# Performance work log

Hardware: AMD Instinct MI355X
Metric: run time of the kernel (lower is better)

Reference implementation:

```python
import jax, jax.numpy as jnp
import numpy as np

PAD = 1  # symmetric spatial padding (pad_H == pad_W enforced by the module)


def setup_inputs() -> dict:
    key = jax.random.key(0)
    k1, k2, k3 = jax.random.split(key, 3)
    N, C, F, H, W, HH, WW = 32, 128, 128, 32, 32, 3, 3
    x = jax.random.normal(k1, (N, C, H, W), dtype=jnp.float32)
    weight = jax.random.normal(k2, (F, C, HH, WW), dtype=jnp.float32) * 0.05
    bias = jax.random.normal(k3, (F,), dtype=jnp.float32) * 0.05
    return {"x": x, "weight": weight, "bias": bias}


def reference(x, weight, bias):
    # Conv2dfft forward, no compression (compress_rate=0, preserve_energy=100,
    # next_power2=False, stride=1, real_fft path).
    N, C, H, W = x.shape
    F, _, HH, WW = weight.shape
    pad = PAD
    out_H = H - HH + 1 + 2 * pad
    out_W = W - WW + 1 + 2 * pad
    HHH = max(out_H, HH)
    WWW = max(out_W, WW)
    init_H = H + 2 * pad + HHH - 1  # full linear-conv FFT size
    init_W = W + 2 * pad + WWW - 1
    # torch_pad(input, (pad_W, pad_W + fft_pad_W, pad_H, pad_H + fft_pad_H))
    xp = jnp.pad(x, ((0, 0), (0, 0), (pad, init_H - pad - H), (pad, init_W - pad - W)))
    # torch_pad(filter, (0, fft_pad_W, 0, fft_pad_H))
    wp = jnp.pad(weight, ((0, 0), (0, 0), (0, init_H - HH), (0, init_W - WW)))
    xf = jnp.fft.rfft2(xp)          # [N, C, init_H, init_W//2+1] complex
    wf = jnp.fft.rfft2(wp)          # [F, C, init_H, init_W//2+1] complex
    # Cross-correlation in frequency domain: xfft * conj(yfft), contracted
    # over input channels C per frequency bin. This is exactly the math of the
    # module's fast_multiply (3-real-mult complex product via matmul) applied
    # to the conjugated filter spectrum.
    of = jnp.einsum('nchw,fchw->nfhw', xf, jnp.conj(wf))
    out = jnp.fft.irfft2(of, s=(init_H, init_W))[..., :out_H, :out_W]
    return out + bias[None, :, None, None]
```

## Files before the change

### kernel.cpp

```cpp
#include <hip/hip_runtime.h>


typedef short bf16x8 __attribute__((ext_vector_type(8)));
typedef short bf16x4 __attribute__((ext_vector_type(4)));
typedef float f32x4  __attribute__((ext_vector_type(4)));

__device__ __forceinline__ short f2bf(float f) {
  unsigned u = __builtin_bit_cast(unsigned, f);
  u = (u + 0x7fffu + ((u >> 16) & 1u)) >> 16;
  return (short)u;
}

__device__ __forceinline__ void gload_lds16(const void* g, void* l) {
  using gptr_t = const __attribute__((address_space(1))) unsigned int*;
  using lptr_t = __attribute__((address_space(3))) unsigned int*;
  __builtin_amdgcn_global_load_lds((gptr_t)(unsigned long long)g,
                                   (lptr_t)(unsigned int)(unsigned long long)l,
                                   16, 0, 0);
}

__global__ __launch_bounds__(256) void conv_wprep(const float* __restrict__ w,
                                                  short* __restrict__ bc2) {
  int tid = blockIdx.x * 256 + threadIdx.x;
  float v = w[tid];
  int f   = tid / 1152;
  int rem = tid - f * 1152;
  int c   = rem / 9;
  int tap = rem - c * 9;
  int p = tap / 3, q = tap - p * 3;
  int grp   = (c >> 5) * 3 + p;
  int fhalf = f >> 6;
  int fblk4 = (f >> 4) & 3;
  int lane  = ((c >> 3) & 3) * 16 + (f & 15);
  int dst = ((((fhalf * 12 + grp) * 3 + q) * 4 + fblk4) * 512) + lane * 8 + (c & 7);
  bc2[dst] = f2bf(v);
}

__global__ __launch_bounds__(256, 2) void conv_main(
    const float* __restrict__ x, const short* __restrict__ bc2,
    const float* __restrict__ bias, float* __restrict__ out) {
  __shared__ __align__(16) short xs[2][6 * 34 * 40];
  __shared__ __align__(16) short afl[2][6144];

  const int t    = threadIdx.x;
  const int lane = t & 63;
  const int wv   = t >> 6;
  const int b     = blockIdx.x;
  const int n_img = b >> 4;
  const int h0    = ((b >> 1) & 7) << 2;
  const int fhalf = b & 1;

  const int l15   = lane & 15;
  const int quad  = lane >> 4;
  const int f_off = fhalf * 64;
  const int s_row = wv;

  const int w_ = t & 31;
  const int g  = t >> 5;
  const float* xb = x + n_img * 128 * 1024;

  const char* bc2b = (const char*)bc2 + fhalf * 147456 + t * 16;

  {
    char* dst = (char*)&afl[0][0] + wv * 1024;
#pragma unroll
    for (int r = 0; r < 3; ++r)
      gload_lds16(bc2b + r * 4096, dst + r * 4096);
  }

  if (t < 192) {
    int buf = t / 96, rem = t % 96;
    int r = rem >> 4, rem2 = rem & 15;
    int colsel = rem2 >> 3, q4 = rem2 & 7;
    *(int2*)&xs[buf][(r * 34 + colsel * 33) * 40 + q4 * 4] = make_int2(0, 0);
  }

  f32x4 acc[4][2] = {};
  float xv[24];

#pragma unroll
  for (int i = 0; i < 6; ++i) {
    int idx = i * 8 + g;
    int r = idx >> 3, cq = idx & 7;
    int hr = h0 - 1 + r;
    bool ok = (unsigned)hr < 32u;
#pragma unroll
    for (int cc = 0; cc < 4; ++cc)
      xv[i * 4 + cc] = ok ? xb[(cq * 4 + cc) * 1024 + hr * 32 + w_] : 0.f;
  }
#pragma unroll
  for (int i = 0; i < 6; ++i) {
    int idx = i * 8 + g;
    int r = idx >> 3, cq = idx & 7;
    bf16x4 v = { f2bf(xv[i*4+0]), f2bf(xv[i*4+1]), f2bf(xv[i*4+2]), f2bf(xv[i*4+3]) };
    *(bf16x4*)&xs[0][(r * 34 + w_ + 1) * 40 + cq * 4] = v;
  }
  __syncthreads();

#pragma unroll
  for (int chunk = 0; chunk < 4; ++chunk) {
#pragma unroll
    for (int p = 0; p < 3; ++p) {
      const int grp = chunk * 3 + p;
      if (grp < 11) {
        const char* src = bc2b + (grp + 1) * 12288;
        char* dst = (char*)&afl[(grp + 1) & 1][0] + wv * 1024;
#pragma unroll
        for (int r = 0; r < 3; ++r)
          gload_lds16(src + r * 4096, dst + r * 4096);
      }
      if (p == 1 && chunk < 3) {
#pragma unroll
        for (int i = 0; i < 6; ++i) {
          int idx = i * 8 + g;
          int r = idx >> 3, cq = idx & 7;
          int hr = h0 - 1 + r;
          bool ok = (unsigned)hr < 32u;
#pragma unroll
          for (int cc = 0; cc < 4; ++cc)
            xv[i * 4 + cc] =
                ok ? xb[((chunk + 1) * 32 + cq * 4 + cc) * 1024 + hr * 32 + w_] : 0.f;
        }
      }
      const short* xbuf = xs[chunk & 1];
      const short* afb  = afl[grp & 1];
      bf16x8 af[12];
#pragma unroll
      for (int q = 0; q < 3; ++q)
#pragma unroll
        for (int mt = 0; mt < 4; ++mt)
          af[q * 4 + mt] = *(const bf16x8*)&afb[(q * 4 + mt) * 512 + lane * 8];
#pragma unroll
      for (int q = 0; q < 3; ++q) {
        bf16x8 bfr[2];
#pragma unroll
        for (int nt = 0; nt < 2; ++nt) {
          int r   = s_row + p;
          int col = nt * 16 + l15 + q;
          bfr[nt] = *(const bf16x8*)&xbuf[(r * 34 + col) * 40 + quad * 8];
        }
#pragma unroll
        for (int mt = 0; mt < 4; ++mt)
#pragma unroll
          for (int nt = 0; nt < 2; ++nt)
            acc[mt][nt] = __builtin_amdgcn_mfma_f32_16x16x32_bf16(
                af[q * 4 + mt], bfr[nt], acc[mt][nt], 0, 0, 0);
      }
      if (p == 2 && chunk < 3) {
#pragma unroll
        for (int i = 0; i < 6; ++i) {
          int idx = i * 8 + g;
          int r = idx >> 3, cq = idx & 7;
          bf16x4 v = { f2bf(xv[i*4+0]), f2bf(xv[i*4+1]), f2bf(xv[i*4+2]), f2bf(xv[i*4+3]) };
          *(bf16x4*)&xs[(chunk + 1) & 1][(r * 34 + w_ + 1) * 40 + cq * 4] = v;
        }
      }
      if (grp < 11) __syncthreads();
    }
  }

  const int h = h0 + s_row;
#pragma unroll
  for (int nt = 0; nt < 2; ++nt) {
    int w_out = nt * 16 + l15;
#pragma unroll
    for (int mt = 0; mt < 4; ++mt) {
#pragma unroll
      for (int reg = 0; reg < 4; ++reg) {
        int f = f_off + mt * 16 + quad * 4 + reg;
        out[(((size_t)n_img * 128 + f) * 32 + h) * 32 + w_out] =
            acc[mt][nt][reg] + bias[f];
      }
    }
  }
}

extern "C" void kernel_launch(void* const* d_in, const int* in_sizes, int n_in,
                              void* d_out, int out_size, void* d_ws, size_t ws_size,
                              hipStream_t stream) {
  const float* x    = (const float*)d_in[0];
  const float* w    = (const float*)d_in[1];
  const float* bias = (const float*)d_in[2];
  float* out = (float*)d_out;
  short* bc2 = (short*)d_ws;

  conv_wprep<<<576, 256, 0, stream>>>(w, bc2);
  conv_main<<<512, 256, 0, stream>>>(x, bc2, bias, out);
}
```

Before: 84.41 us.

## Retile conv to 16-row x 32-filter blocks with resident weights and row reuse

Each block now covers 16 output rows and 32 filters with 512 threads, where it previously covered 4 rows and 64 filters with 256. The whole 32-filter weight slice (about 72KB bf16) is loaded into LDS once up front, replacing the per-group double-buffered weight streaming. Each wave computes two output rows and reuses the loaded input rows across the 3 vertical taps, which cuts LDS reads per MFMA. The input tile is now single-buffered, so each of the 4 channel chunks needs two barriers. Larger LDS use (about 120KB) limits occupancy, and the grid shrinks to 256 blocks.

```diff
diff --git a/kernel.cpp b/kernel.cpp
--- a/kernel.cpp
+++ b/kernel.cpp
@@ -29,58 +29,57 @@
   int tap = rem - c * 9;
   int p = tap / 3, q = tap - p * 3;
   int grp   = (c >> 5) * 3 + p;
-  int fhalf = f >> 6;
-  int fblk4 = (f >> 4) & 3;
+  int fq    = f >> 5;
+  int fblk2 = (f >> 4) & 1;
   int lane  = ((c >> 3) & 3) * 16 + (f & 15);
-  int dst = ((((fhalf * 12 + grp) * 3 + q) * 4 + fblk4) * 512) + lane * 8 + (c & 7);
+  int dst = ((((fq * 12 + grp) * 3 + q) * 2 + fblk2) * 512) + lane * 8 + (c & 7);
   bc2[dst] = f2bf(v);
 }
 
-__global__ __launch_bounds__(256, 2) void conv_main(
+__global__ __launch_bounds__(512, 2) void conv_main(
     const float* __restrict__ x, const short* __restrict__ bc2,
     const float* __restrict__ bias, float* __restrict__ out) {
-  __shared__ __align__(16) short xs[2][6 * 34 * 40];
-  __shared__ __align__(16) short afl[2][6144];
+  __shared__ __align__(16) short xs[18 * 34 * 40];
+  __shared__ __align__(16) short afl[36864];
 
   const int t    = threadIdx.x;
   const int lane = t & 63;
   const int wv   = t >> 6;
   const int b     = blockIdx.x;
-  const int n_img = b >> 4;
-  const int h0    = ((b >> 1) & 7) << 2;
-  const int fhalf = b & 1;
+  const int n_img = b >> 3;
+  const int hhalf = (b >> 2) & 1;
+  const int fq    = b & 3;
+  const int h0    = hhalf << 4;
 
-  const int l15   = lane & 15;
-  const int quad  = lane >> 4;
-  const int f_off = fhalf * 64;
-  const int s_row = wv;
+  const int l15    = lane & 15;
+  const int quad   = lane >> 4;
+  const int f_off  = fq << 5;
+  const int r_base = wv << 1;
 
   const int w_ = t & 31;
   const int g  = t >> 5;
   const float* xb = x + n_img * 128 * 1024;
 
-  const char* bc2b = (const char*)bc2 + fhalf * 147456 + t * 16;
-
   {
-    char* dst = (char*)&afl[0][0] + wv * 1024;
+    const char* src = (const char*)bc2 + fq * 73728 + t * 16;
+    char* dst = (char*)&afl[0] + wv * 1024;
 #pragma unroll
-    for (int r = 0; r < 3; ++r)
-      gload_lds16(bc2b + r * 4096, dst + r * 4096);
+    for (int r = 0; r < 9; ++r)
+      gload_lds16(src + r * 8192, dst + r * 8192);
   }
 
-  if (t < 192) {
-    int buf = t / 96, rem = t % 96;
-    int r = rem >> 4, rem2 = rem & 15;
-    int colsel = rem2 >> 3, q4 = rem2 & 7;
-    *(int2*)&xs[buf][(r * 34 + colsel * 33) * 40 + q4 * 4] = make_int2(0, 0);
+  if (t < 288) {
+    int r = t >> 4, rem = t & 15;
+    int colsel = rem >> 3, q4 = rem & 7;
+    *(int2*)&xs[(r * 34 + colsel * 33) * 40 + q4 * 4] = make_int2(0, 0);
   }
 
-  f32x4 acc[4][2] = {};
-  float xv[24];
+  f32x4 acc[2][2][2] = {};
+  float xv[36];
 
 #pragma unroll
-  for (int i = 0; i < 6; ++i) {
-    int idx = i * 8 + g;
+  for (int i = 0; i < 9; ++i) {
+    int idx = i * 16 + g;
     int r = idx >> 3, cq = idx & 7;
     int hr = h0 - 1 + r;
     bool ok = (unsigned)hr < 32u;
@@ -89,87 +88,81 @@
       xv[i * 4 + cc] = ok ? xb[(cq * 4 + cc) * 1024 + hr * 32 + w_] : 0.f;
   }
 #pragma unroll
-  for (int i = 0; i < 6; ++i) {
-    int idx = i * 8 + g;
+  for (int i = 0; i < 9; ++i) {
+    int idx = i * 16 + g;
     int r = idx >> 3, cq = idx & 7;
     bf16x4 v = { f2bf(xv[i*4+0]), f2bf(xv[i*4+1]), f2bf(xv[i*4+2]), f2bf(xv[i*4+3]) };
-    *(bf16x4*)&xs[0][(r * 34 + w_ + 1) * 40 + cq * 4] = v;
+    *(bf16x4*)&xs[(r * 34 + w_ + 1) * 40 + cq * 4] = v;
   }
   __syncthreads();
 
 #pragma unroll
   for (int chunk = 0; chunk < 4; ++chunk) {
+    if (chunk < 3) {
 #pragma unroll
-    for (int p = 0; p < 3; ++p) {
-      const int grp = chunk * 3 + p;
-      if (grp < 11) {
-        const char* src = bc2b + (grp + 1) * 12288;
-        char* dst = (char*)&afl[(grp + 1) & 1][0] + wv * 1024;
+      for (int i = 0; i < 9; ++i) {
+        int idx = i * 16 + g;
+        int r = idx >> 3, cq = idx & 7;
+        int hr = h0 - 1 + r;
+        bool ok = (unsigned)hr < 32u;
 #pragma unroll
-        for (int r = 0; r < 3; ++r)
-          gload_lds16(src + r * 4096, dst + r * 4096);
+        for (int cc = 0; cc < 4; ++cc)
+          xv[i * 4 + cc] =
+              ok ? xb[((chunk + 1) * 32 + cq * 4 + cc) * 1024 + hr * 32 + w_] : 0.f;
       }
-      if (p == 1 && chunk < 3) {
+    }
+    const int grp0 = chunk * 3;
 #pragma unroll
-        for (int i = 0; i < 6; ++i) {
-          int idx = i * 8 + g;
-          int r = idx >> 3, cq = idx & 7;
-          int hr = h0 - 1 + r;
-          bool ok = (unsigned)hr < 32u;
+    for (int q = 0; q < 3; ++q) {
+      bf16x8 bfr[4][2];
 #pragma unroll
-          for (int cc = 0; cc < 4; ++cc)
-            xv[i * 4 + cc] =
-                ok ? xb[((chunk + 1) * 32 + cq * 4 + cc) * 1024 + hr * 32 + w_] : 0.f;
-        }
+      for (int rr = 0; rr < 4; ++rr)
+#pragma unroll
+        for (int nt = 0; nt < 2; ++nt)
+          bfr[rr][nt] = *(const bf16x8*)
+              &xs[((r_base + rr) * 34 + nt * 16 + l15 + q) * 40 + quad * 8];
+#pragma unroll
+      for (int p = 0; p < 3; ++p) {
+        bf16x8 af0 = *(const bf16x8*)&afl[(((grp0 + p) * 3 + q) * 2 + 0) * 512 + lane * 8];
+        bf16x8 af1 = *(const bf16x8*)&afl[(((grp0 + p) * 3 + q) * 2 + 1) * 512 + lane * 8];
+#pragma unroll
+        for (int d = 0; d < 2; ++d)
+#pragma unroll
+          for (int nt = 0; nt < 2; ++nt) {
+            acc[d][0][nt] = __builtin_amdgcn_mfma_f32_16x16x32_bf16(
+                af0, bfr[p + d][nt], acc[d][0][nt], 0, 0, 0);
+            acc[d][1][nt] = __builtin_amdgcn_mfma_f32_16x16x32_bf16(
+                af1, bfr[p + d][nt], acc[d][1][nt], 0, 0, 0);
+          }
       }
-      const short* xbuf = xs[chunk & 1];
-      const short* afb  = afl[grp & 1];
-      bf16x8 af[12];
+    }
+    if (chunk < 3) {
+      __syncthreads();
 #pragma unroll
-      for (int q = 0; q < 3; ++q)
-#pragma unroll
-        for (int mt = 0; mt < 4; ++mt)
-          af[q * 4 + mt] = *(const bf16x8*)&afb[(q * 4 + mt) * 512 + lane * 8];
-#pragma unroll
-      for (int q = 0; q < 3; ++q) {
-        bf16x8 bfr[2];
-#pragma unroll
-        for (int nt = 0; nt < 2; ++nt) {
-          int r   = s_row + p;
-          int col = nt * 16 + l15 + q;
-          bfr[nt] = *(const bf16x8*)&xbuf[(r * 34 + col) * 40 + quad * 8];
-        }
-#pragma unroll
-        for (int mt = 0; mt < 4; ++mt)
-#pragma unroll
-          for (int nt = 0; nt < 2; ++nt)
-            acc[mt][nt] = __builtin_amdgcn_mfma_f32_16x16x32_bf16(
-                af[q * 4 + mt], bfr[nt], acc[mt][nt], 0, 0, 0);
+      for (int i = 0; i < 9; ++i) {
+        int idx = i * 16 + g;
+        int r = idx >> 3, cq = idx & 7;
+        bf16x4 v = { f2bf(xv[i*4+0]), f2bf(xv[i*4+1]), f2bf(xv[i*4+2]), f2bf(xv[i*4+3]) };
+        *(bf16x4*)&xs[(r * 34 + w_ + 1) * 40 + cq * 4] = v;
       }
-      if (p == 2 && chunk < 3) {
-#pragma unroll
-        for (int i = 0; i < 6; ++i) {
-          int idx = i * 8 + g;
-          int r = idx >> 3, cq = idx & 7;
-          bf16x4 v = { f2bf(xv[i*4+0]), f2bf(xv[i*4+1]), f2bf(xv[i*4+2]), f2bf(xv[i*4+3]) };
-          *(bf16x4*)&xs[(chunk + 1) & 1][(r * 34 + w_ + 1) * 40 + cq * 4] = v;
-        }
-      }
-      if (grp < 11) __syncthreads();
+      __syncthreads();
     }
   }
 
-  const int h = h0 + s_row;
 #pragma unroll
-  for (int nt = 0; nt < 2; ++nt) {
-    int w_out = nt * 16 + l15;
+  for (int d = 0; d < 2; ++d) {
+    const int h = h0 + r_base + d;
 #pragma unroll
-    for (int mt = 0; mt < 4; ++mt) {
+    for (int nt = 0; nt < 2; ++nt) {
+      int w_out = nt * 16 + l15;
 #pragma unroll
-      for (int reg = 0; reg < 4; ++reg) {
-        int f = f_off + mt * 16 + quad * 4 + reg;
-        out[(((size_t)n_img * 128 + f) * 32 + h) * 32 + w_out] =
-            acc[mt][nt][reg] + bias[f];
+      for (int mt = 0; mt < 2; ++mt) {
+#pragma unroll
+        for (int reg = 0; reg < 4; ++reg) {
+          int f = f_off + mt * 16 + quad * 4 + reg;
+          out[(((size_t)n_img * 128 + f) * 32 + h) * 32 + w_out] =
+              acc[d][mt][nt][reg] + bias[f];
+        }
       }
     }
   }
@@ -185,5 +178,5 @@
   short* bc2 = (short*)d_ws;
 
   conv_wprep<<<576, 256, 0, stream>>>(w, bc2);
-  conv_main<<<512, 256, 0, stream>>>(x, bc2, bias, out);
+  conv_main<<<256, 512, 0, stream>>>(x, bc2, bias, out);
 }
```

Result: slower. 91.03 us (+7.8%).
